# Performance work log

Measured on AMD Instinct MI355X. Metric: run time of the kernel, lower is better.

The kernel has to match this reference:

```python
import jax, jax.numpy as jnp
import numpy as np

B, N, D, H, DK, DV = 2, 2048, 1024, 16, 64, 64
NEG = -1000000000.0
EPS = 1e-6


def setup_inputs() -> dict:
    key = jax.random.key(0)
    ks = jax.random.split(key, 8)
    s = 0.02
    return {
        "q": jax.random.normal(ks[0], (B, N, D), jnp.float32),
        "k": jax.random.normal(ks[1], (B, N, D), jnp.float32),
        "v": jax.random.normal(ks[2], (B, N, D), jnp.float32),
        "attn_mask": jnp.ones((B, N, N), jnp.int32),
        "Wq": jax.random.normal(ks[3], (D, H * DK), jnp.float32) * s,
        "Wk": jax.random.normal(ks[4], (D, H * DK), jnp.float32) * s,
        "Wv": jax.random.normal(ks[5], (D, H * DV), jnp.float32) * s,
        "Wo": jax.random.normal(ks[6], (H * DV, D), jnp.float32) * s,
        "gamma": jnp.ones((D,), jnp.float32),
        "beta": jnp.zeros((D,), jnp.float32),
    }


def reference(q, k, v, attn_mask, Wq, Wk, Wv, Wo, gamma, beta):
    b, n, _ = q.shape
    residual = q
    # project and split heads: (b, h, n, dk)
    qh = (q @ Wq).reshape(b, n, H, DK).transpose(0, 2, 1, 3)
    kh = (k @ Wk).reshape(b, n, H, DK).transpose(0, 2, 1, 3)
    vh = (v @ Wv).reshape(b, n, H, DV).transpose(0, 2, 1, 3)
    temperature = DK ** 0.5
    scores = jnp.einsum('bhnd,bhmd->bhnm', qh / temperature, kh)
    # external mask (masked where mask == 0), broadcast over heads
    scores = jnp.where(attn_mask[:, None, :, :] == 0, NEG, scores)
    # built-in causal mask (strictly upper triangle)
    causal = jnp.triu(jnp.ones((n, n), dtype=bool), k=1)
    scores = jnp.where(causal, NEG, scores)
    attn = jax.nn.softmax(scores, axis=-1)
    out = jnp.einsum('bhnm,bhmd->bnhd', attn, vh).reshape(b, n, H * DV)
    out = out @ Wo + residual
    # LayerNorm(eps=1e-6)
    mean = out.mean(-1, keepdims=True)
    var = ((out - mean) ** 2).mean(-1, keepdims=True)
    out = (out - mean) / jnp.sqrt(var + EPS) * gamma + beta
    return out, attn
```

## Files before the change

kernel.cpp:

```cpp
#include <hip/hip_runtime.h>
#include <hip/hip_bf16.h>
#include <stdint.h>

#define B_ 2
#define N_ 2048
#define D_ 1024
#define H_ 16
#define MM 4096
#define NN 1024
#define KK 1024

typedef __bf16 bf16;
typedef __bf16 bf16x8 __attribute__((ext_vector_type(8)));
typedef float f32x4 __attribute__((ext_vector_type(4)));

struct __align__(8) bf4 { bf16 v[4]; };

#define LDS_STRIDE 144
#define LOG2E 1.44269504088896340736f

#define GLDS(gp, lp)                                                     \
    __builtin_amdgcn_global_load_lds(                                    \
        (const __attribute__((address_space(1))) void*)(gp),             \
        (__attribute__((address_space(3))) void*)(lp), 16, 0, 0)

__global__ __launch_bounds__(256) void k_cvt3(const float* __restrict__ q,
                                              const float* __restrict__ k,
                                              const float* __restrict__ v,
                                              bf16* __restrict__ qb,
                                              bf16* __restrict__ kb,
                                              bf16* __restrict__ vb) {
    const int z = blockIdx.y;
    const float* s = z == 0 ? q : z == 1 ? k : v;
    bf16* d = z == 0 ? qb : z == 1 ? kb : vb;
    size_t i = ((size_t)blockIdx.x * 256 + threadIdx.x) * 8;
    f32x4 a = *(const f32x4*)(s + i);
    f32x4 b = *(const f32x4*)(s + i + 4);
    bf16x8 o;
#pragma unroll
    for (int j = 0; j < 4; ++j) { o[j] = (bf16)a[j]; o[4 + j] = (bf16)b[j]; }
    *(bf16x8*)(d + i) = o;
}

__global__ void k_wtt4(const float* __restrict__ Wq, const float* __restrict__ Wk,
                       const float* __restrict__ Wv, const float* __restrict__ Wo,
                       bf16* __restrict__ WqT, bf16* __restrict__ WkT,
                       bf16* __restrict__ WvT, bf16* __restrict__ WoT) {
    const int z = blockIdx.z;
    const float* W = z == 0 ? Wq : z == 1 ? Wk : z == 2 ? Wv : Wo;
    bf16* Wt = z == 0 ? WqT : z == 1 ? WkT : z == 2 ? WvT : WoT;
    __shared__ float t[32][33];
    int bx = blockIdx.x * 32, by = blockIdx.y * 32;
    int tx = threadIdx.x, ty = threadIdx.y;
#pragma unroll
    for (int j = 0; j < 32; j += 8)
        t[ty + j][tx] = W[(size_t)(by + ty + j) * 1024 + bx + tx];
    __syncthreads();
#pragma unroll
    for (int j = 0; j < 32; j += 8)
        Wt[(size_t)(bx + ty + j) * 1024 + by + tx] = (bf16)t[tx][ty + j];
}

__global__ __launch_bounds__(256) void k_bits(const int* __restrict__ mask,
                                              uint32_t* __restrict__ bits) {
    size_t flat = (size_t)blockIdx.x * 256 + threadIdx.x;
    int col = (int)(flat & (N_ - 1));
    int row = (int)((flat >> 11) & (N_ - 1));
    bool ok = (mask[flat] != 0) && (col <= row);
    unsigned long long bal = __ballot(ok);
    if ((threadIdx.x & 63) == 0)
        *(unsigned long long*)(bits + (flat >> 5)) = bal;
}

__device__ __forceinline__ void mm_core(const bf16* __restrict__ A,
                                        const bf16* __restrict__ Bt,
                                        int bm0, int bn0,
                                        bf16* As, bf16* Bs,
                                        f32x4 (&acc)[4][4]) {
    const int tid = threadIdx.x, w = tid >> 6, lane = tid & 63;
    const int g = lane >> 4, li = lane & 15;
    const int wr = w >> 1, wc = w & 1;

    f32x4 zz = {0.f, 0.f, 0.f, 0.f};
#pragma unroll
    for (int mf = 0; mf < 4; ++mf)
#pragma unroll
        for (int nf = 0; nf < 4; ++nf) acc[mf][nf] = zz;

    auto stage = [&](int k0) {
#pragma unroll
        for (int c = 0; c < 4; ++c) {
            int ch = c * 256 + tid;
            int r = ch >> 3, cl = ch & 7;
            GLDS(A + (size_t)(bm0 + r) * KK + k0 + cl * 8,
                 As + ((size_t)c * 256 + w * 64) * 8);
        }
#pragma unroll
        for (int c = 0; c < 4; ++c) {
            int ch = c * 256 + tid;
            int r = ch >> 3, cl = ch & 7;
            GLDS(Bt + (size_t)(bn0 + r) * KK + k0 + cl * 8,
                 Bs + ((size_t)c * 256 + w * 64) * 8);
        }
    };

    stage(0);
    for (int s = 0; s < KK / 64; ++s) {
        __syncthreads();
#pragma unroll
        for (int kk = 0; kk < 2; ++kk) {
            bf16x8 af[4], bfr[4];
#pragma unroll
            for (int i = 0; i < 4; ++i) {
                af[i] = *(const bf16x8*)(As + (wr * 64 + i * 16 + li) * 64 + kk * 32 + g * 8);
                bfr[i] = *(const bf16x8*)(Bs + (wc * 64 + i * 16 + li) * 64 + kk * 32 + g * 8);
            }
#pragma unroll
            for (int mf = 0; mf < 4; ++mf)
#pragma unroll
                for (int nf = 0; nf < 4; ++nf)
                    acc[mf][nf] = __builtin_amdgcn_mfma_f32_16x16x32_bf16(
                        af[mf], bfr[nf], acc[mf][nf], 0, 0, 0);
        }
        __syncthreads();
        if (s + 1 < KK / 64) stage((s + 1) * 64);
    }
}

__global__ __launch_bounds__(256) void k_proj(const bf16* __restrict__ qb,
                                              const bf16* __restrict__ kb,
                                              const bf16* __restrict__ vb,
                                              const bf16* __restrict__ WqT,
                                              const bf16* __restrict__ WkT,
                                              const bf16* __restrict__ WvT,
                                              bf16* __restrict__ Qh,
                                              bf16* __restrict__ Kh,
                                              bf16* __restrict__ Vt) {
    __shared__ __align__(16) bf16 As[128 * 64];
    __shared__ __align__(16) bf16 Bs[128 * 64];
    const int z = blockIdx.y;
    const bf16* A = z == 0 ? qb : z == 1 ? kb : vb;
    const bf16* Bt = z == 0 ? WqT : z == 1 ? WkT : WvT;
    int bid = blockIdx.x;
    int swz = (bid & 7) * 32 + (bid >> 3);
    int bm0 = (swz >> 3) * 128, bn0 = (swz & 7) * 128;

    f32x4 acc[4][4];
    mm_core(A, Bt, bm0, bn0, As, Bs, acc);

    const int tid = threadIdx.x, w = tid >> 6, lane = tid & 63;
    const int g = lane >> 4, li = lane & 15;
    const int wr = w >> 1, wc = w & 1;
    const float scale = (z == 0) ? 0.125f * LOG2E : 1.0f;

    if (z < 2) {
        bf16* C = (z == 0) ? Qh : Kh;
#pragma unroll
        for (int mf = 0; mf < 4; ++mf)
#pragma unroll
            for (int nf = 0; nf < 4; ++nf) {
                int m0 = bm0 + wr * 64 + mf * 16 + g * 4;
                int n = bn0 + wc * 64 + nf * 16 + li;
#pragma unroll
                for (int r = 0; r < 4; ++r)
                    C[(size_t)(m0 + r) * NN + n] = (bf16)(acc[mf][nf][r] * scale);
            }
    } else {
#pragma unroll
        for (int mf = 0; mf < 4; ++mf)
#pragma unroll
            for (int nf = 0; nf < 4; ++nf) {
                int m0 = bm0 + wr * 64 + mf * 16 + g * 4;
                int n = bn0 + wc * 64 + nf * 16 + li;
                int bq = m0 >> 11, tok = m0 & (N_ - 1);
                int hh = n >> 6, dv = n & 63;
                bf4 val;
#pragma unroll
                for (int r = 0; r < 4; ++r) val.v[r] = (bf16)acc[mf][nf][r];
                *(bf4*)(Vt + ((size_t)((bq * H_ + hh) * 64 + dv)) * N_ + tok) = val;
            }
    }
}

__global__ __launch_bounds__(256) void k_out(const bf16* __restrict__ Ob,
                                             const bf16* __restrict__ WoT,
                                             float* __restrict__ outp,
                                             const float* __restrict__ resid) {
    __shared__ __align__(16) bf16 As[128 * 64];
    __shared__ __align__(16) bf16 Bs[128 * 64];
    int bid = blockIdx.x;
    int swz = (bid & 7) * 32 + (bid >> 3);
    int bm0 = (swz >> 3) * 128, bn0 = (swz & 7) * 128;

    f32x4 acc[4][4];
    mm_core(Ob, WoT, bm0, bn0, As, Bs, acc);

    const int tid = threadIdx.x, w = tid >> 6, lane = tid & 63;
    const int g = lane >> 4, li = lane & 15;
    const int wr = w >> 1, wc = w & 1;
#pragma unroll
    for (int mf = 0; mf < 4; ++mf)
#pragma unroll
        for (int nf = 0; nf < 4; ++nf) {
            int m0 = bm0 + wr * 64 + mf * 16 + g * 4;
            int n = bn0 + wc * 64 + nf * 16 + li;
#pragma unroll
            for (int r = 0; r < 4; ++r) {
                size_t ix = (size_t)(m0 + r) * NN + n;
                outp[ix] = acc[mf][nf][r] + resid[ix];
            }
        }
}

__global__ __launch_bounds__(256) void k_attn(const bf16* __restrict__ Qh,
                                              const bf16* __restrict__ Kh,
                                              const bf16* __restrict__ Vt,
                                              const uint32_t* __restrict__ bits,
                                              float* __restrict__ attnp,
                                              bf16* __restrict__ Ob) {
    __shared__ __align__(16) char Qs[64 * LDS_STRIDE];
    __shared__ __align__(16) char Ks[64 * LDS_STRIDE];
    __shared__ __align__(16) char Vs[64 * LDS_STRIDE];
    __shared__ __align__(16) char Ps[64 * LDS_STRIDE];
    const int tid = threadIdx.x, lane = tid & 63, w = tid >> 6;
    const int g = lane >> 4, li = lane & 15;
    const int p = blockIdx.x, h = blockIdx.y, b = blockIdx.z;
    const int srow = tid >> 3, sc = tid & 7;
    const int myrow = w * 16 + li;

    const size_t kbase = ((size_t)b * N_) * D_ + h * 64;
    const size_t vbase = ((size_t)(b * H_ + h) * 64) * N_;
    f32x4 zz = {0.f, 0.f, 0.f, 0.f};

    for (int half = 0; half < 2; ++half) {
        const int qt = half ? (31 - p) : p;
        const int i0 = qt << 6;
        const size_t abase = (((size_t)b * H_ + h) * N_ + i0) * (size_t)N_;

        __syncthreads();
        {
            const char* qsrc = (const char*)Qh +
                (kbase + (size_t)(i0 + srow) * D_ + sc * 8) * 2;
            bf16x8 t0 = *(const bf16x8*)qsrc;
            bf16x8 t1 = *(const bf16x8*)(qsrc + (size_t)32 * D_ * 2);
            *(bf16x8*)(Qs + srow * LDS_STRIDE + sc * 16) = t0;
            *(bf16x8*)(Qs + (srow + 32) * LDS_STRIDE + sc * 16) = t1;
        }
        const uint32_t* mrow = bits + (((size_t)b * N_ + i0 + myrow) << 6);

        float m = -1e30f, l = 0.f;
        bf16x8 ka, kb2, va, vb2;
        {
            const char* ks = (const char*)Kh + (kbase + (size_t)srow * D_ + sc * 8) * 2;
            ka = *(const bf16x8*)ks;
            kb2 = *(const bf16x8*)(ks + (size_t)32 * D_ * 2);
        }
        for (int jt = 0; jt <= qt; ++jt) {
            __syncthreads();
            *(bf16x8*)(Ks + srow * LDS_STRIDE + sc * 16) = ka;
            *(bf16x8*)(Ks + (srow + 32) * LDS_STRIDE + sc * 16) = kb2;
            {
                int jn = (jt < qt) ? jt + 1 : qt;
                const char* ks = (const char*)Kh +
                    (kbase + (size_t)(jn * 64 + srow) * D_ + sc * 8) * 2;
                ka = *(const bf16x8*)ks;
                kb2 = *(const bf16x8*)(ks + (size_t)32 * D_ * 2);
            }
            uint2 mw = *(const uint2*)(mrow + (jt << 1));
            __syncthreads();

            f32x4 s[4];
#pragma unroll
            for (int mf = 0; mf < 4; ++mf) s[mf] = zz;
#pragma unroll
            for (int kk = 0; kk < 2; ++kk) {
                const int kb = kk * 64 + (g << 4);
                bf16x8 qf = *(const bf16x8*)(Qs + myrow * LDS_STRIDE + kb);
#pragma unroll
                for (int mf = 0; mf < 4; ++mf) {
                    bf16x8 kf = *(const bf16x8*)(Ks + (mf * 16 + li) * LDS_STRIDE + kb);
                    s[mf] = __builtin_amdgcn_mfma_f32_16x16x32_bf16(kf, qf, s[mf], 0, 0, 0);
                }
            }
            float tmax = m;
#pragma unroll
            for (int mf = 0; mf < 4; ++mf) {
                uint32_t wsel = (mf < 2) ? mw.x : mw.y;
#pragma unroll
                for (int r = 0; r < 4; ++r) {
                    int sh = (mf & 1) * 16 + g * 4 + r;
                    float xv = ((wsel >> sh) & 1) ? s[mf][r] : -1e9f;
                    s[mf][r] = xv;
                    tmax = fmaxf(tmax, xv);
                }
            }
            tmax = fmaxf(tmax, __shfl_xor(tmax, 16));
            tmax = fmaxf(tmax, __shfl_xor(tmax, 32));
            float ps = 0.f;
#pragma unroll
            for (int mf = 0; mf < 4; ++mf)
#pragma unroll
                for (int r = 0; r < 4; ++r) ps += exp2f(s[mf][r] - tmax);
            ps += __shfl_xor(ps, 16);
            ps += __shfl_xor(ps, 32);
            l = l * exp2f(m - tmax) + ps;
            m = tmax;
        }
        const float ml = m + __log2f(l);

        f32x4 oacc[4];
#pragma unroll
        for (int nf = 0; nf < 4; ++nf) oacc[nf] = zz;

        {
            const char* ks = (const char*)Kh + (kbase + (size_t)srow * D_ + sc * 8) * 2;
            ka = *(const bf16x8*)ks;
            kb2 = *(const bf16x8*)(ks + (size_t)32 * D_ * 2);
            const char* vs = (const char*)Vt + (vbase + (size_t)srow * N_ + sc * 8) * 2;
            va = *(const bf16x8*)vs;
            vb2 = *(const bf16x8*)(vs + (size_t)32 * N_ * 2);
        }
        for (int jt = 0; jt <= qt; ++jt) {
            __syncthreads();
            *(bf16x8*)(Ks + srow * LDS_STRIDE + sc * 16) = ka;
            *(bf16x8*)(Ks + (srow + 32) * LDS_STRIDE + sc * 16) = kb2;
            *(bf16x8*)(Vs + srow * LDS_STRIDE + sc * 16) = va;
            *(bf16x8*)(Vs + (srow + 32) * LDS_STRIDE + sc * 16) = vb2;
            {
                int jn = (jt < qt) ? jt + 1 : qt;
                const char* ks = (const char*)Kh +
                    (kbase + (size_t)(jn * 64 + srow) * D_ + sc * 8) * 2;
                ka = *(const bf16x8*)ks;
                kb2 = *(const bf16x8*)(ks + (size_t)32 * D_ * 2);
                const char* vs = (const char*)Vt +
                    (vbase + (size_t)srow * N_ + jn * 64 + sc * 8) * 2;
                va = *(const bf16x8*)vs;
                vb2 = *(const bf16x8*)(vs + (size_t)32 * N_ * 2);
            }
            uint2 mw = *(const uint2*)(mrow + (jt << 1));
            __syncthreads();

            f32x4 s[4];
#pragma unroll
            for (int mf = 0; mf < 4; ++mf) s[mf] = zz;
#pragma unroll
            for (int kk = 0; kk < 2; ++kk) {
                const int kb = kk * 64 + (g << 4);
                bf16x8 qf = *(const bf16x8*)(Qs + myrow * LDS_STRIDE + kb);
#pragma unroll
                for (int mf = 0; mf < 4; ++mf) {
                    bf16x8 kf = *(const bf16x8*)(Ks + (mf * 16 + li) * LDS_STRIDE + kb);
                    s[mf] = __builtin_amdgcn_mfma_f32_16x16x32_bf16(kf, qf, s[mf], 0, 0, 0);
                }
            }

#pragma unroll
            for (int mf = 0; mf < 4; ++mf) {
                uint32_t wsel = (mf < 2) ? mw.x : mw.y;
#pragma unroll
                for (int r = 0; r < 4; ++r) {
                    int sh = (mf & 1) * 16 + g * 4 + r;
                    float xv = ((wsel >> sh) & 1) ? s[mf][r] : -1e9f;
                    s[mf][r] = exp2f(xv - ml);
                }
                __builtin_nontemporal_store(s[mf],
                    (f32x4*)(attnp + abase + (size_t)myrow * N_ + (jt << 6) + mf * 16 + g * 4));
                bf4 pk;
#pragma unroll
                for (int r = 0; r < 4; ++r) pk.v[r] = (bf16)s[mf][r];
                *(bf4*)(Ps + myrow * LDS_STRIDE + (mf * 16 + g * 4) * 2) = pk;
            }
#pragma unroll
            for (int kk = 0; kk < 2; ++kk) {
                const int kb = kk * 64 + (g << 4);
                bf16x8 pf = *(const bf16x8*)(Ps + myrow * LDS_STRIDE + kb);
#pragma unroll
                for (int nf = 0; nf < 4; ++nf) {
                    bf16x8 vf = *(const bf16x8*)(Vs + (nf * 16 + li) * LDS_STRIDE + kb);
                    oacc[nf] = __builtin_amdgcn_mfma_f32_16x16x32_bf16(pf, vf, oacc[nf], 0, 0, 0);
                }
            }
        }
#pragma unroll
        for (int nf = 0; nf < 4; ++nf)
#pragma unroll
            for (int r = 0; r < 4; ++r) {
                int gi = i0 + w * 16 + g * 4 + r;
                Ob[((size_t)(b * N_ + gi)) * D_ + h * 64 + nf * 16 + li] = (bf16)oacc[nf][r];
            }
        int zc0 = i0 + 64;
        if (zc0 < N_) {
            int r = tid >> 2, tc = tid & 3;
            f32x4 z = zz;
            for (int c = zc0 + tc * 4; c < N_; c += 16)
                __builtin_nontemporal_store(z, (f32x4*)(attnp + abase + (size_t)r * N_ + c));
        }
    }
}

__global__ __launch_bounds__(256) void k_ln(float* __restrict__ out,
                                            const float* __restrict__ gamma,
                                            const float* __restrict__ beta) {
    const int row = blockIdx.x, t = threadIdx.x, lane = t & 63, w = t >> 6;
    float* p = out + (size_t)row * D_;
    f32x4 x = *(const f32x4*)(p + t * 4);
    float s = x[0] + x[1] + x[2] + x[3];
    float s2 = x[0] * x[0] + x[1] * x[1] + x[2] * x[2] + x[3] * x[3];
#pragma unroll
    for (int o = 1; o < 64; o <<= 1) {
        s += __shfl_xor(s, o);
        s2 += __shfl_xor(s2, o);
    }
    __shared__ float r1[4], r2[4];
    if (lane == 0) { r1[w] = s; r2[w] = s2; }
    __syncthreads();
    s = r1[0] + r1[1] + r1[2] + r1[3];
    s2 = r2[0] + r2[1] + r2[2] + r2[3];
    float mean = s * (1.f / D_);
    float var = s2 * (1.f / D_) - mean * mean;
    float rstd = rsqrtf(var + 1e-6f);
    f32x4 gv = *(const f32x4*)(gamma + t * 4);
    f32x4 bv = *(const f32x4*)(beta + t * 4);
    f32x4 y;
#pragma unroll
    for (int c = 0; c < 4; ++c) y[c] = (x[c] - mean) * rstd * gv[c] + bv[c];
    *(f32x4*)(p + t * 4) = y;
}

extern "C" void kernel_launch(void* const* d_in, const int* in_sizes, int n_in,
                              void* d_out, int out_size, void* d_ws,
                              size_t ws_size, hipStream_t stream) {
    (void)in_sizes; (void)n_in; (void)out_size; (void)ws_size;
    const float* q = (const float*)d_in[0];
    const float* k = (const float*)d_in[1];
    const float* v = (const float*)d_in[2];
    const int* msk = (const int*)d_in[3];
    const float* Wq = (const float*)d_in[4];
    const float* Wk = (const float*)d_in[5];
    const float* Wv = (const float*)d_in[6];
    const float* Wo = (const float*)d_in[7];
    const float* gamma = (const float*)d_in[8];
    const float* beta = (const float*)d_in[9];

    float* outp = (float*)d_out;
    float* attnp = outp + (size_t)B_ * N_ * D_;

    const size_t U = (size_t)B_ * N_ * D_;
    const size_t W1 = (size_t)D_ * D_;
    bf16* ws = (bf16*)d_ws;
    bf16* qb = ws;   ws += U;
    bf16* kb = ws;   ws += U;
    bf16* vb = ws;   ws += U;
    bf16* WqT = ws;  ws += W1;
    bf16* WkT = ws;  ws += W1;
    bf16* WvT = ws;  ws += W1;
    bf16* WoT = ws;  ws += W1;
    bf16* Qh = ws;   ws += U;
    bf16* Kh = ws;   ws += U;
    bf16* Vt = ws;   ws += U;
    bf16* Ob = ws;   ws += U;
    uint32_t* bits = (uint32_t*)ws;

    k_cvt3<<<dim3(U / 8 / 256, 3), 256, 0, stream>>>(q, k, v, qb, kb, vb);
    k_wtt4<<<dim3(32, 32, 4), dim3(32, 8), 0, stream>>>(Wq, Wk, Wv, Wo, WqT, WkT, WvT, WoT);
    k_bits<<<(size_t)B_ * N_ * N_ / 256, 256, 0, stream>>>(msk, bits);

    k_proj<<<dim3(256, 3), 256, 0, stream>>>(qb, kb, vb, WqT, WkT, WvT, Qh, Kh, Vt);

    k_attn<<<dim3(16, H_, B_), 256, 0, stream>>>(Qh, Kh, Vt, bits, attnp, Ob);

    k_out<<<256, 256, 0, stream>>>(Ob, WoT, outp, q);

    k_ln<<<B_ * N_, 256, 0, stream>>>(outp, gamma, beta);
}
```

Measured before the change: 306.8 us.

## Fuse fp32-to-bf16 input conversion into projection GEMM and shrink attention query tiles

Removes the separate conversion kernel: the projection GEMM now loads fp32 q/k/v straight into registers, converts to bf16 and writes to padded LDS, prefetching the next k-slice. This drops a full read and write of three bf16 activation buffers. The attention kernel now uses 32-row query tiles with 128-thread blocks and twice as many blocks, with a finer causal bound and adjusted zero-fill start, for better balance and occupancy. The cost is that the A operand is now staged through registers instead of async global-to-LDS loads, and each K/V tile is reloaded more often because query tiles are smaller.

```diff
diff --git a/kernel.cpp b/kernel.cpp
--- a/kernel.cpp
+++ b/kernel.cpp
@@ -23,24 +23,6 @@
     __builtin_amdgcn_global_load_lds(                                    \
         (const __attribute__((address_space(1))) void*)(gp),             \
         (__attribute__((address_space(3))) void*)(lp), 16, 0, 0)
-
-__global__ __launch_bounds__(256) void k_cvt3(const float* __restrict__ q,
-                                              const float* __restrict__ k,
-                                              const float* __restrict__ v,
-                                              bf16* __restrict__ qb,
-                                              bf16* __restrict__ kb,
-                                              bf16* __restrict__ vb) {
-    const int z = blockIdx.y;
-    const float* s = z == 0 ? q : z == 1 ? k : v;
-    bf16* d = z == 0 ? qb : z == 1 ? kb : vb;
-    size_t i = ((size_t)blockIdx.x * 256 + threadIdx.x) * 8;
-    f32x4 a = *(const f32x4*)(s + i);
-    f32x4 b = *(const f32x4*)(s + i + 4);
-    bf16x8 o;
-#pragma unroll
-    for (int j = 0; j < 4; ++j) { o[j] = (bf16)a[j]; o[4 + j] = (bf16)b[j]; }
-    *(bf16x8*)(d + i) = o;
-}
 
 __global__ void k_wtt4(const float* __restrict__ Wq, const float* __restrict__ Wk,
                        const float* __restrict__ Wv, const float* __restrict__ Wo,
@@ -72,87 +54,95 @@
         *(unsigned long long*)(bits + (flat >> 5)) = bal;
 }
 
-__device__ __forceinline__ void mm_core(const bf16* __restrict__ A,
-                                        const bf16* __restrict__ Bt,
-                                        int bm0, int bn0,
-                                        bf16* As, bf16* Bs,
-                                        f32x4 (&acc)[4][4]) {
-    const int tid = threadIdx.x, w = tid >> 6, lane = tid & 63;
-    const int g = lane >> 4, li = lane & 15;
-    const int wr = w >> 1, wc = w & 1;
-
-    f32x4 zz = {0.f, 0.f, 0.f, 0.f};
-#pragma unroll
-    for (int mf = 0; mf < 4; ++mf)
-#pragma unroll
-        for (int nf = 0; nf < 4; ++nf) acc[mf][nf] = zz;
-
-    auto stage = [&](int k0) {
-#pragma unroll
-        for (int c = 0; c < 4; ++c) {
-            int ch = c * 256 + tid;
-            int r = ch >> 3, cl = ch & 7;
-            GLDS(A + (size_t)(bm0 + r) * KK + k0 + cl * 8,
-                 As + ((size_t)c * 256 + w * 64) * 8);
-        }
-#pragma unroll
-        for (int c = 0; c < 4; ++c) {
-            int ch = c * 256 + tid;
-            int r = ch >> 3, cl = ch & 7;
-            GLDS(Bt + (size_t)(bn0 + r) * KK + k0 + cl * 8,
-                 Bs + ((size_t)c * 256 + w * 64) * 8);
-        }
-    };
-
-    stage(0);
-    for (int s = 0; s < KK / 64; ++s) {
-        __syncthreads();
-#pragma unroll
-        for (int kk = 0; kk < 2; ++kk) {
-            bf16x8 af[4], bfr[4];
-#pragma unroll
-            for (int i = 0; i < 4; ++i) {
-                af[i] = *(const bf16x8*)(As + (wr * 64 + i * 16 + li) * 64 + kk * 32 + g * 8);
-                bfr[i] = *(const bf16x8*)(Bs + (wc * 64 + i * 16 + li) * 64 + kk * 32 + g * 8);
-            }
-#pragma unroll
-            for (int mf = 0; mf < 4; ++mf)
-#pragma unroll
-                for (int nf = 0; nf < 4; ++nf)
-                    acc[mf][nf] = __builtin_amdgcn_mfma_f32_16x16x32_bf16(
-                        af[mf], bfr[nf], acc[mf][nf], 0, 0, 0);
-        }
-        __syncthreads();
-        if (s + 1 < KK / 64) stage((s + 1) * 64);
-    }
-}
-
-__global__ __launch_bounds__(256) void k_proj(const bf16* __restrict__ qb,
-                                              const bf16* __restrict__ kb,
-                                              const bf16* __restrict__ vb,
+__global__ __launch_bounds__(256) void k_proj(const float* __restrict__ qf,
+                                              const float* __restrict__ kf,
+                                              const float* __restrict__ vf,
                                               const bf16* __restrict__ WqT,
                                               const bf16* __restrict__ WkT,
                                               const bf16* __restrict__ WvT,
                                               bf16* __restrict__ Qh,
                                               bf16* __restrict__ Kh,
                                               bf16* __restrict__ Vt) {
-    __shared__ __align__(16) bf16 As[128 * 64];
+    __shared__ __align__(16) bf16 As[128 * 72];
     __shared__ __align__(16) bf16 Bs[128 * 64];
     const int z = blockIdx.y;
-    const bf16* A = z == 0 ? qb : z == 1 ? kb : vb;
+    const float* A = z == 0 ? qf : z == 1 ? kf : vf;
     const bf16* Bt = z == 0 ? WqT : z == 1 ? WkT : WvT;
     int bid = blockIdx.x;
     int swz = (bid & 7) * 32 + (bid >> 3);
     int bm0 = (swz >> 3) * 128, bn0 = (swz & 7) * 128;
 
-    f32x4 acc[4][4];
-    mm_core(A, Bt, bm0, bn0, As, Bs, acc);
-
     const int tid = threadIdx.x, w = tid >> 6, lane = tid & 63;
     const int g = lane >> 4, li = lane & 15;
     const int wr = w >> 1, wc = w & 1;
+
+    f32x4 zz = {0.f, 0.f, 0.f, 0.f};
+    f32x4 acc[4][4];
+#pragma unroll
+    for (int mf = 0; mf < 4; ++mf)
+#pragma unroll
+        for (int nf = 0; nf < 4; ++nf) acc[mf][nf] = zz;
+
+    f32x4 pa[4][2];
+    auto issueA = [&](int k0) {
+#pragma unroll
+        for (int c = 0; c < 4; ++c) {
+            int ch = c * 256 + tid;
+            int r = ch >> 3, cl = ch & 7;
+            const float* s = A + (size_t)(bm0 + r) * KK + k0 + cl * 8;
+            pa[c][0] = *(const f32x4*)s;
+            pa[c][1] = *(const f32x4*)(s + 4);
+        }
+    };
+    auto writeA = [&]() {
+#pragma unroll
+        for (int c = 0; c < 4; ++c) {
+            int ch = c * 256 + tid;
+            int r = ch >> 3, cl = ch & 7;
+            bf16x8 t;
+#pragma unroll
+            for (int j = 0; j < 4; ++j) {
+                t[j] = (bf16)pa[c][0][j];
+                t[4 + j] = (bf16)pa[c][1][j];
+            }
+            *(bf16x8*)(As + (size_t)r * 72 + cl * 8) = t;
+        }
+    };
+    auto stageB = [&](int k0) {
+#pragma unroll
+        for (int c = 0; c < 4; ++c) {
+            int ch = c * 256 + tid;
+            int r = ch >> 3, cl = ch & 7;
+            GLDS(Bt + (size_t)(bn0 + r) * KK + k0 + cl * 8,
+                 Bs + ((size_t)c * 256 + w * 64) * 8);
+        }
+    };
+
+    issueA(0);
+    for (int s = 0; s < KK / 64; ++s) {
+        __syncthreads();
+        writeA();
+        stageB(s * 64);
+        if (s + 1 < KK / 64) issueA((s + 1) * 64);
+        __syncthreads();
+#pragma unroll
+        for (int kk = 0; kk < 2; ++kk) {
+            bf16x8 af[4], bfr[4];
+#pragma unroll
+            for (int i = 0; i < 4; ++i) {
+                af[i] = *(const bf16x8*)(As + (wr * 64 + i * 16 + li) * 72 + kk * 32 + g * 8);
+                bfr[i] = *(const bf16x8*)(Bs + (wc * 64 + i * 16 + li) * 64 + kk * 32 + g * 8);
+            }
+#pragma unroll
+            for (int mf = 0; mf < 4; ++mf)
+#pragma unroll
+                for (int nf = 0; nf < 4; ++nf)
+                    acc[mf][nf] = __builtin_amdgcn_mfma_f32_16x16x32_bf16(
+                        af[mf], bfr[nf], acc[mf][nf], 0, 0, 0);
+        }
+    }
+
     const float scale = (z == 0) ? 0.125f * LOG2E : 1.0f;
-
     if (z < 2) {
         bf16* C = (z == 0) ? Qh : Kh;
 #pragma unroll
@@ -192,12 +182,55 @@
     int swz = (bid & 7) * 32 + (bid >> 3);
     int bm0 = (swz >> 3) * 128, bn0 = (swz & 7) * 128;
 
-    f32x4 acc[4][4];
-    mm_core(Ob, WoT, bm0, bn0, As, Bs, acc);
-
     const int tid = threadIdx.x, w = tid >> 6, lane = tid & 63;
     const int g = lane >> 4, li = lane & 15;
     const int wr = w >> 1, wc = w & 1;
+
+    f32x4 zz = {0.f, 0.f, 0.f, 0.f};
+    f32x4 acc[4][4];
+#pragma unroll
+    for (int mf = 0; mf < 4; ++mf)
+#pragma unroll
+        for (int nf = 0; nf < 4; ++nf) acc[mf][nf] = zz;
+
+    auto stage = [&](int k0) {
+#pragma unroll
+        for (int c = 0; c < 4; ++c) {
+            int ch = c * 256 + tid;
+            int r = ch >> 3, cl = ch & 7;
+            GLDS(Ob + (size_t)(bm0 + r) * KK + k0 + cl * 8,
+                 As + ((size_t)c * 256 + w * 64) * 8);
+        }
+#pragma unroll
+        for (int c = 0; c < 4; ++c) {
+            int ch = c * 256 + tid;
+            int r = ch >> 3, cl = ch & 7;
+            GLDS(WoT + (size_t)(bn0 + r) * KK + k0 + cl * 8,
+                 Bs + ((size_t)c * 256 + w * 64) * 8);
+        }
+    };
+
+    stage(0);
+    for (int s = 0; s < KK / 64; ++s) {
+        __syncthreads();
+#pragma unroll
+        for (int kk = 0; kk < 2; ++kk) {
+            bf16x8 af[4], bfr[4];
+#pragma unroll
+            for (int i = 0; i < 4; ++i) {
+                af[i] = *(const bf16x8*)(As + (wr * 64 + i * 16 + li) * 64 + kk * 32 + g * 8);
+                bfr[i] = *(const bf16x8*)(Bs + (wc * 64 + i * 16 + li) * 64 + kk * 32 + g * 8);
+            }
+#pragma unroll
+            for (int mf = 0; mf < 4; ++mf)
+#pragma unroll
+                for (int nf = 0; nf < 4; ++nf)
+                    acc[mf][nf] = __builtin_amdgcn_mfma_f32_16x16x32_bf16(
+                        af[mf], bfr[nf], acc[mf][nf], 0, 0, 0);
+        }
+        __syncthreads();
+        if (s + 1 < KK / 64) stage((s + 1) * 64);
+    }
 #pragma unroll
     for (int mf = 0; mf < 4; ++mf)
 #pragma unroll
@@ -212,16 +245,16 @@
         }
 }
 
-__global__ __launch_bounds__(256) void k_attn(const bf16* __restrict__ Qh,
+__global__ __launch_bounds__(128) void k_attn(const bf16* __restrict__ Qh,
                                               const bf16* __restrict__ Kh,
                                               const bf16* __restrict__ Vt,
                                               const uint32_t* __restrict__ bits,
                                               float* __restrict__ attnp,
                                               bf16* __restrict__ Ob) {
-    __shared__ __align__(16) char Qs[64 * LDS_STRIDE];
+    __shared__ __align__(16) char Qs[32 * LDS_STRIDE];
     __shared__ __align__(16) char Ks[64 * LDS_STRIDE];
     __shared__ __align__(16) char Vs[64 * LDS_STRIDE];
-    __shared__ __align__(16) char Ps[64 * LDS_STRIDE];
+    __shared__ __align__(16) char Ps[32 * LDS_STRIDE];
     const int tid = threadIdx.x, lane = tid & 63, w = tid >> 6;
     const int g = lane >> 4, li = lane & 15;
     const int p = blockIdx.x, h = blockIdx.y, b = blockIdx.z;
@@ -232,40 +265,55 @@
     const size_t vbase = ((size_t)(b * H_ + h) * 64) * N_;
     f32x4 zz = {0.f, 0.f, 0.f, 0.f};
 
+    bf16x8 kr[4], vr[4];
+    auto loadK = [&](int jt) {
+        const char* ks = (const char*)Kh +
+            (kbase + (size_t)(jt * 64 + srow) * D_ + sc * 8) * 2;
+#pragma unroll
+        for (int i = 0; i < 4; ++i)
+            kr[i] = *(const bf16x8*)(ks + (size_t)(16 * i) * D_ * 2);
+    };
+    auto loadV = [&](int jt) {
+        const char* vs = (const char*)Vt +
+            (vbase + (size_t)srow * N_ + jt * 64 + sc * 8) * 2;
+#pragma unroll
+        for (int i = 0; i < 4; ++i)
+            vr[i] = *(const bf16x8*)(vs + (size_t)(16 * i) * N_ * 2);
+    };
+    auto writeK = [&]() {
+#pragma unroll
+        for (int i = 0; i < 4; ++i)
+            *(bf16x8*)(Ks + (srow + 16 * i) * LDS_STRIDE + sc * 16) = kr[i];
+    };
+    auto writeV = [&]() {
+#pragma unroll
+        for (int i = 0; i < 4; ++i)
+            *(bf16x8*)(Vs + (srow + 16 * i) * LDS_STRIDE + sc * 16) = vr[i];
+    };
+
     for (int half = 0; half < 2; ++half) {
-        const int qt = half ? (31 - p) : p;
-        const int i0 = qt << 6;
-        const size_t abase = (((size_t)b * H_ + h) * N_ + i0) * (size_t)N_;
+        const int sl = half ? (63 - p) : p;
+        const int qs0 = sl << 5;
+        const int jt_max = sl >> 1;
+        const size_t abase = (((size_t)b * H_ + h) * N_ + qs0) * (size_t)N_;
 
         __syncthreads();
         {
             const char* qsrc = (const char*)Qh +
-                (kbase + (size_t)(i0 + srow) * D_ + sc * 8) * 2;
+                (kbase + (size_t)(qs0 + srow) * D_ + sc * 8) * 2;
             bf16x8 t0 = *(const bf16x8*)qsrc;
-            bf16x8 t1 = *(const bf16x8*)(qsrc + (size_t)32 * D_ * 2);
+            bf16x8 t1 = *(const bf16x8*)(qsrc + (size_t)16 * D_ * 2);
             *(bf16x8*)(Qs + srow * LDS_STRIDE + sc * 16) = t0;
-            *(bf16x8*)(Qs + (srow + 32) * LDS_STRIDE + sc * 16) = t1;
-        }
-        const uint32_t* mrow = bits + (((size_t)b * N_ + i0 + myrow) << 6);
+            *(bf16x8*)(Qs + (srow + 16) * LDS_STRIDE + sc * 16) = t1;
+        }
+        const uint32_t* mrow = bits + (((size_t)b * N_ + qs0 + myrow) << 6);
 
         float m = -1e30f, l = 0.f;
-        bf16x8 ka, kb2, va, vb2;
-        {
-            const char* ks = (const char*)Kh + (kbase + (size_t)srow * D_ + sc * 8) * 2;
-            ka = *(const bf16x8*)ks;
-            kb2 = *(const bf16x8*)(ks + (size_t)32 * D_ * 2);
-        }
-        for (int jt = 0; jt <= qt; ++jt) {
+        loadK(0);
+        for (int jt = 0; jt <= jt_max; ++jt) {
             __syncthreads();
-            *(bf16x8*)(Ks + srow * LDS_STRIDE + sc * 16) = ka;
-            *(bf16x8*)(Ks + (srow + 32) * LDS_STRIDE + sc * 16) = kb2;
-            {
-                int jn = (jt < qt) ? jt + 1 : qt;
-                const char* ks = (const char*)Kh +
-                    (kbase + (size_t)(jn * 64 + srow) * D_ + sc * 8) * 2;
-                ka = *(const bf16x8*)ks;
-                kb2 = *(const bf16x8*)(ks + (size_t)32 * D_ * 2);
-            }
+            writeK();
+            if (jt < jt_max) loadK(jt + 1);
             uint2 mw = *(const uint2*)(mrow + (jt << 1));
             __syncthreads();
 
@@ -275,11 +323,11 @@
 #pragma unroll
             for (int kk = 0; kk < 2; ++kk) {
                 const int kb = kk * 64 + (g << 4);
-                bf16x8 qf = *(const bf16x8*)(Qs + myrow * LDS_STRIDE + kb);
+                bf16x8 qv = *(const bf16x8*)(Qs + myrow * LDS_STRIDE + kb);
 #pragma unroll
                 for (int mf = 0; mf < 4; ++mf) {
-                    bf16x8 kf = *(const bf16x8*)(Ks + (mf * 16 + li) * LDS_STRIDE + kb);
-                    s[mf] = __builtin_amdgcn_mfma_f32_16x16x32_bf16(kf, qf, s[mf], 0, 0, 0);
+                    bf16x8 kv = *(const bf16x8*)(Ks + (mf * 16 + li) * LDS_STRIDE + kb);
+                    s[mf] = __builtin_amdgcn_mfma_f32_16x16x32_bf16(kv, qv, s[mf], 0, 0, 0);
                 }
             }
             float tmax = m;
@@ -312,31 +360,13 @@
 #pragma unroll
         for (int nf = 0; nf < 4; ++nf) oacc[nf] = zz;
 
-        {
-            const char* ks = (const char*)Kh + (kbase + (size_t)srow * D_ + sc * 8) * 2;
-            ka = *(const bf16x8*)ks;
-            kb2 = *(const bf16x8*)(ks + (size_t)32 * D_ * 2);
-            const char* vs = (const char*)Vt + (vbase + (size_t)srow * N_ + sc * 8) * 2;
-            va = *(const bf16x8*)vs;
-            vb2 = *(const bf16x8*)(vs + (size_t)32 * N_ * 2);
-        }
-        for (int jt = 0; jt <= qt; ++jt) {
+        loadK(0);
+        loadV(0);
+        for (int jt = 0; jt <= jt_max; ++jt) {
             __syncthreads();
-            *(bf16x8*)(Ks + srow * LDS_STRIDE + sc * 16) = ka;
-            *(bf16x8*)(Ks + (srow + 32) * LDS_STRIDE + sc * 16) = kb2;
-            *(bf16x8*)(Vs + srow * LDS_STRIDE + sc * 16) = va;
-            *(bf16x8*)(Vs + (srow + 32) * LDS_STRIDE + sc * 16) = vb2;
-            {
-                int jn = (jt < qt) ? jt + 1 : qt;
-                const char* ks = (const char*)Kh +
-                    (kbase + (size_t)(jn * 64 + srow) * D_ + sc * 8) * 2;
-                ka = *(const bf16x8*)ks;
-                kb2 = *(const bf16x8*)(ks + (size_t)32 * D_ * 2);
-                const char* vs = (const char*)Vt +
-                    (vbase + (size_t)srow * N_ + jn * 64 + sc * 8) * 2;
-                va = *(const bf16x8*)vs;
-                vb2 = *(const bf16x8*)(vs + (size_t)32 * N_ * 2);
-            }
+            writeK();
+            writeV();
+            if (jt < jt_max) { loadK(jt + 1); loadV(jt + 1); }
             uint2 mw = *(const uint2*)(mrow + (jt << 1));
             __syncthreads();
 
@@ -346,11 +376,11 @@
 #pragma unroll
             for (int kk = 0; kk < 2; ++kk) {
                 const int kb = kk * 64 + (g << 4);
-                bf16x8 qf = *(const bf16x8*)(Qs + myrow * LDS_STRIDE + kb);
+                bf16x8 qv = *(const bf16x8*)(Qs + myrow * LDS_STRIDE + kb);
 #pragma unroll
                 for (int mf = 0; mf < 4; ++mf) {
-                    bf16x8 kf = *(const bf16x8*)(Ks + (mf * 16 + li) * LDS_STRIDE + kb);
-                    s[mf] = __builtin_amdgcn_mfma_f32_16x16x32_bf16(kf, qf, s[mf], 0, 0, 0);
+                    bf16x8 kv = *(const bf16x8*)(Ks + (mf * 16 + li) * LDS_STRIDE + kb);
+                    s[mf] = __builtin_amdgcn_mfma_f32_16x16x32_bf16(kv, qv, s[mf], 0, 0, 0);
                 }
             }
 
@@ -376,8 +406,8 @@
                 bf16x8 pf = *(const bf16x8*)(Ps + myrow * LDS_STRIDE + kb);
 #pragma unroll
                 for (int nf = 0; nf < 4; ++nf) {
-                    bf16x8 vf = *(const bf16x8*)(Vs + (nf * 16 + li) * LDS_STRIDE + kb);
-                    oacc[nf] = __builtin_amdgcn_mfma_f32_16x16x32_bf16(pf, vf, oacc[nf], 0, 0, 0);
+                    bf16x8 vv = *(const bf16x8*)(Vs + (nf * 16 + li) * LDS_STRIDE + kb);
+                    oacc[nf] = __builtin_amdgcn_mfma_f32_16x16x32_bf16(pf, vv, oacc[nf], 0, 0, 0);
                 }
             }
         }
@@ -385,10 +415,10 @@
         for (int nf = 0; nf < 4; ++nf)
 #pragma unroll
             for (int r = 0; r < 4; ++r) {
-                int gi = i0 + w * 16 + g * 4 + r;
+                int gi = qs0 + w * 16 + g * 4 + r;
                 Ob[((size_t)(b * N_ + gi)) * D_ + h * 64 + nf * 16 + li] = (bf16)oacc[nf][r];
             }
-        int zc0 = i0 + 64;
+        int zc0 = (jt_max + 1) << 6;
         if (zc0 < N_) {
             int r = tid >> 2, tc = tid & 3;
             f32x4 z = zz;
@@ -448,9 +478,6 @@
     const size_t U = (size_t)B_ * N_ * D_;
     const size_t W1 = (size_t)D_ * D_;
     bf16* ws = (bf16*)d_ws;
-    bf16* qb = ws;   ws += U;
-    bf16* kb = ws;   ws += U;
-    bf16* vb = ws;   ws += U;
     bf16* WqT = ws;  ws += W1;
     bf16* WkT = ws;  ws += W1;
     bf16* WvT = ws;  ws += W1;
@@ -461,13 +488,12 @@
     bf16* Ob = ws;   ws += U;
     uint32_t* bits = (uint32_t*)ws;
 
-    k_cvt3<<<dim3(U / 8 / 256, 3), 256, 0, stream>>>(q, k, v, qb, kb, vb);
     k_wtt4<<<dim3(32, 32, 4), dim3(32, 8), 0, stream>>>(Wq, Wk, Wv, Wo, WqT, WkT, WvT, WoT);
     k_bits<<<(size_t)B_ * N_ * N_ / 256, 256, 0, stream>>>(msk, bits);
 
-    k_proj<<<dim3(256, 3), 256, 0, stream>>>(qb, kb, vb, WqT, WkT, WvT, Qh, Kh, Vt);
-
-    k_attn<<<dim3(16, H_, B_), 256, 0, stream>>>(Qh, Kh, Vt, bits, attnp, Ob);
+    k_proj<<<dim3(256, 3), 256, 0, stream>>>(q, k, v, WqT, WkT, WvT, Qh, Kh, Vt);
+
+    k_attn<<<dim3(32, H_, B_), 128, 0, stream>>>(Qh, Kh, Vt, bits, attnp, Ob);
 
     k_out<<<256, 256, 0, stream>>>(Ob, WoT, outp, q);
 
```

After: 325.7 us. 6.2% more time.
